# Kernel tuning notes

Measured on AMD Instinct MI355X. Metric: run time of the kernel, lower is better.

Reference implementation:

```python
import jax, jax.numpy as jnp
import numpy as np


def setup_inputs() -> dict:
    key = jax.random.key(0)
    ks = jax.random.split(key, 5)
    Bsz, T, d = 8, 2048, 1024
    x = jax.random.normal(ks[0], (Bsz, T, d), dtype=jnp.float32)
    W_in = jax.random.normal(ks[1], (d, d), dtype=jnp.float32) * (1.0 / np.sqrt(d))
    b_in = jnp.zeros((d,), dtype=jnp.float32)
    log_A = -jnp.ones((d,), dtype=jnp.float32)  # keras Constant(-1.0) init
    B_vec = jax.random.normal(ks[2], (d,), dtype=jnp.float32) * 0.05  # keras random_normal stddev
    C = jax.random.normal(ks[3], (d, d), dtype=jnp.float32) * 0.05
    D = jnp.zeros((d,), dtype=jnp.float32)
    return {"x": x, "W_in": W_in, "b_in": b_in, "log_A": log_A, "B_vec": B_vec, "C": C, "D": D}


def reference(x, W_in, b_in, log_A, B_vec, C, D):
    # u = in_proj(x)
    u = jnp.einsum('btd,de->bte', x, W_in) + b_in            # [B,T,d]
    A = -jnp.exp(log_A)                                       # [d]
    # linear recurrence h_t = h_{t-1} * A + u_t * B, h_0 = 0
    # expressed as an associative scan over pairs (a_t, b_t):
    #   (a1,b1) o (a2,b2) = (a1*a2, b1*a2 + b2)
    b = u * B_vec                                             # [B,T,d]
    a = jnp.broadcast_to(A, b.shape)                          # [B,T,d]

    def combine(e1, e2):
        a1, b1 = e1
        a2, b2 = e2
        return (a1 * a2, b1 * a2 + b2)

    _, h_seq = jax.lax.associative_scan(combine, (a, b), axis=1)  # h_t, [B,T,d]
    y = jnp.einsum('bts,sd->btd', h_seq, C)
    return y + x * D
```

## Files before the change

kernel.cpp:

```cpp
#include <hip/hip_runtime.h>
#include <hip/hip_bf16.h>

typedef unsigned short ushort_t;
typedef __bf16 bf16x8 __attribute__((ext_vector_type(8)));
typedef float f32x4 __attribute__((ext_vector_type(4)));

#define BM 128
#define BN 128
#define BK 64

__device__ __forceinline__ float bf2f(ushort_t u) {
    union { unsigned int i; float f; } x; x.i = ((unsigned int)u) << 16; return x.f;
}
__device__ __forceinline__ ushort_t f2bf(float f) {
    __hip_bfloat16 h = __float2bfloat16(f);
    return *(ushort_t*)&h;
}
__device__ __forceinline__ void async16(const void* g, void* l) {
    __builtin_amdgcn_global_load_lds((const __attribute__((address_space(1))) void*)g,
                                     (__attribute__((address_space(3))) void*)l, 16, 0, 0);
}

__global__ void prep_fused(const float* __restrict__ x, const float* __restrict__ W_in,
                           const float* __restrict__ C, const float* __restrict__ Bv,
                           __hip_bfloat16* __restrict__ xb, __hip_bfloat16* __restrict__ Wpt,
                           __hip_bfloat16* __restrict__ Ct) {
    int bid = blockIdx.x;
    if (bid < 16384) {
        size_t idx = ((size_t)bid * 256 + threadIdx.x) * 4;
        float4 v = *(const float4*)(x + idx);
        ushort4 ov;
        ov.x = f2bf(v.x); ov.y = f2bf(v.y); ov.z = f2bf(v.z); ov.w = f2bf(v.w);
        *(ushort4*)((ushort_t*)xb + idx) = ov;
        return;
    }
    __shared__ float tile[32][33];
    const float* in;
    __hip_bfloat16* out;
    bool do_scale;
    int lid;
    if (bid < 17408) { lid = bid - 16384; in = W_in; out = Wpt; do_scale = true; }
    else             { lid = bid - 17408; in = C;    out = Ct;  do_scale = false; }
    int bx = (lid & 31) * 32;
    int by = (lid >> 5) * 32;
    int tx = threadIdx.x & 31, ty = threadIdx.x >> 5;
    #pragma unroll
    for (int i = 0; i < 32; i += 8)
        tile[ty + i][tx] = in[(size_t)(by + ty + i) * 1024 + bx + tx];
    __syncthreads();
    #pragma unroll
    for (int i = 0; i < 32; i += 8) {
        int n = bx + ty + i;
        int k = by + tx;
        float s = do_scale ? Bv[n] : 1.0f;
        out[(size_t)n * 1024 + k] = __float2bfloat16(tile[tx][ty + i] * s);
    }
}

template <int EPI>
__global__ __launch_bounds__(256) void gemm_bt(
    const __hip_bfloat16* __restrict__ Ab, const __hip_bfloat16* __restrict__ Btb,
    int M, int N, int K,
    const float* __restrict__ b_in, const float* __restrict__ Bv,
    __hip_bfloat16* __restrict__ out_bf,
    const __hip_bfloat16* __restrict__ xres_bf, const float* __restrict__ Dvec,
    float* __restrict__ out_f) {
    const int tid  = threadIdx.x;
    const int wave = tid >> 6;
    const int lane = tid & 63;
    const int quad = lane >> 4;
    const int lr   = lane & 15;
    const int wm   = wave >> 1;
    const int wn   = wave & 1;

    const int lin   = blockIdx.y * gridDim.x + blockIdx.x;
    const int xcd   = lin & 7;
    const int local = lin >> 3;
    const int m_blk = xcd * 16 + (local >> 3);
    const int n_blk = local & 7;
    const int m0 = m_blk * BM;
    const int n0 = n_blk * BN;

    __shared__ __align__(16) ushort_t sA[BM * BK];
    __shared__ __align__(16) ushort_t sB[BN * BK];

    const ushort_t* A  = (const ushort_t*)Ab;
    const ushort_t* Bt = (const ushort_t*)Btb;

    f32x4 acc[4][4];
    #pragma unroll
    for (int i = 0; i < 4; ++i)
        #pragma unroll
        for (int j = 0; j < 4; ++j)
            #pragma unroll
            for (int r = 0; r < 4; ++r) acc[i][j][r] = 0.0f;

    const int row8 = lane >> 3;
    const int schunk = (lane & 7) ^ row8;
    const int ldcol = schunk * 8;
    for (int k0 = 0; k0 < K; k0 += BK) {
        __syncthreads();
        #pragma unroll
        for (int j = 0; j < 4; ++j) {
            int c = j * 4 + wave;
            int row = c * 8 + row8;
            const ushort_t* gA = A + (size_t)(m0 + row) * K + k0 + ldcol;
            async16(gA, &sA[c * 512]);
            const ushort_t* gB = Bt + (size_t)(n0 + row) * K + k0 + ldcol;
            async16(gB, &sB[c * 512]);
        }
        __syncthreads();
        #pragma unroll
        for (int kk = 0; kk < BK; kk += 32) {
            const int ck = (kk >> 3) + quad;
            const int pc = (ck ^ (lr & 7)) * 8;
            bf16x8 af[4], bfr[4];
            #pragma unroll
            for (int i = 0; i < 4; ++i)
                af[i] = *(const bf16x8*)&sA[(wm * 64 + i * 16 + lr) * BK + pc];
            #pragma unroll
            for (int j = 0; j < 4; ++j)
                bfr[j] = *(const bf16x8*)&sB[(wn * 64 + j * 16 + lr) * BK + pc];
            #pragma unroll
            for (int i = 0; i < 4; ++i)
                #pragma unroll
                for (int j = 0; j < 4; ++j)
                    acc[i][j] = __builtin_amdgcn_mfma_f32_16x16x32_bf16(af[i], bfr[j], acc[i][j], 0, 0, 0);
        }
    }

    #pragma unroll
    for (int i = 0; i < 4; ++i) {
        int row = m0 + wm * 64 + i * 16 + quad * 4;
        #pragma unroll
        for (int j = 0; j < 4; ++j) {
            int col = n0 + wn * 64 + j * 16 + lr;
            if constexpr (EPI == 0) {
                float bs = b_in[col] * Bv[col];
                #pragma unroll
                for (int r = 0; r < 4; ++r)
                    out_bf[(size_t)(row + r) * N + col] = __float2bfloat16(acc[i][j][r] + bs);
            } else {
                float dv = Dvec[col];
                #pragma unroll
                for (int r = 0; r < 4; ++r) {
                    float xv = bf2f(((const ushort_t*)xres_bf)[(size_t)(row + r) * N + col]);
                    out_f[(size_t)(row + r) * N + col] = acc[i][j][r] + xv * dv;
                }
            }
        }
    }
}

#define SCH 32
__global__ void scan_kernel(const __hip_bfloat16* __restrict__ b, __hip_bfloat16* __restrict__ h,
                            const float* __restrict__ logA, int T, int DD) {
    int c0 = (blockIdx.z * 256 + threadIdx.x) * 2;
    int q  = blockIdx.x;
    int bb = blockIdx.y;
    float2 la = *(const float2*)(logA + c0);
    float a0 = -__expf(la.x), a1 = -__expf(la.y);
    float a0_2 = a0 * a0,   a1_2 = a1 * a1;
    float a0_3 = a0_2 * a0, a1_3 = a1_2 * a1;
    float a0_4 = a0_2 * a0_2, a1_4 = a1_2 * a1_2;
    int ts = q * SCH;
    size_t base = (size_t)bb * T * DD + c0;
    float h0 = 0.f, h1 = 0.f;
    if (ts > 0) {
        const ushort_t* wp = (const ushort_t*)b + base + (size_t)(ts - 32) * DD;
        #pragma unroll
        for (int t = 0; t < 32; t += 4) {
            ushort2 v0 = *(const ushort2*)(wp);
            ushort2 v1 = *(const ushort2*)(wp + DD);
            ushort2 v2 = *(const ushort2*)(wp + 2 * (size_t)DD);
            ushort2 v3 = *(const ushort2*)(wp + 3 * (size_t)DD);
            wp += 4 * (size_t)DD;
            float s0 = fmaf(a0_3, bf2f(v0.x), fmaf(a0_2, bf2f(v1.x), fmaf(a0, bf2f(v2.x), bf2f(v3.x))));
            float s1 = fmaf(a1_3, bf2f(v0.y), fmaf(a1_2, bf2f(v1.y), fmaf(a1, bf2f(v2.y), bf2f(v3.y))));
            h0 = fmaf(a0_4, h0, s0);
            h1 = fmaf(a1_4, h1, s1);
        }
    }
    const ushort_t* bp = (const ushort_t*)b + base + (size_t)ts * DD;
    ushort_t* hp = (ushort_t*)h + base + (size_t)ts * DD;
    #pragma unroll
    for (int t = 0; t < SCH; t += 4) {
        ushort2 v0 = *(const ushort2*)(bp);
        ushort2 v1 = *(const ushort2*)(bp + DD);
        ushort2 v2 = *(const ushort2*)(bp + 2 * (size_t)DD);
        ushort2 v3 = *(const ushort2*)(bp + 3 * (size_t)DD);
        bp += 4 * (size_t)DD;
        ushort2 o;
        h0 = fmaf(a0, h0, bf2f(v0.x)); h1 = fmaf(a1, h1, bf2f(v0.y));
        o.x = f2bf(h0); o.y = f2bf(h1); *(ushort2*)hp = o;
        h0 = fmaf(a0, h0, bf2f(v1.x)); h1 = fmaf(a1, h1, bf2f(v1.y));
        o.x = f2bf(h0); o.y = f2bf(h1); *(ushort2*)(hp + DD) = o;
        h0 = fmaf(a0, h0, bf2f(v2.x)); h1 = fmaf(a1, h1, bf2f(v2.y));
        o.x = f2bf(h0); o.y = f2bf(h1); *(ushort2*)(hp + 2 * (size_t)DD) = o;
        h0 = fmaf(a0, h0, bf2f(v3.x)); h1 = fmaf(a1, h1, bf2f(v3.y));
        o.x = f2bf(h0); o.y = f2bf(h1); *(ushort2*)(hp + 3 * (size_t)DD) = o;
        hp += 4 * (size_t)DD;
    }
}

extern "C" void kernel_launch(void* const* d_in, const int* in_sizes, int n_in,
                              void* d_out, int out_size, void* d_ws, size_t ws_size,
                              hipStream_t stream) {
    const float* x    = (const float*)d_in[0];
    const float* W_in = (const float*)d_in[1];
    const float* b_in = (const float*)d_in[2];
    const float* logA = (const float*)d_in[3];
    const float* Bv   = (const float*)d_in[4];
    const float* C    = (const float*)d_in[5];
    const float* Dv   = (const float*)d_in[6];
    float* out = (float*)d_out;

    const int Bsz = 8, T = 2048, d = 1024;
    const int M = Bsz * T;

    char* w = (char*)d_ws;
    __hip_bfloat16* xb   = (__hip_bfloat16*)w;
    __hip_bfloat16* Wpt  = xb + (size_t)M * d;
    __hip_bfloat16* Ct   = Wpt + (size_t)d * d;
    __hip_bfloat16* bbuf = Ct + (size_t)d * d;
    __hip_bfloat16* hbuf = bbuf + (size_t)M * d;

    prep_fused<<<16384 + 2048, 256, 0, stream>>>(x, W_in, C, Bv, xb, Wpt, Ct);

    gemm_bt<0><<<dim3(d / BN, M / BM), 256, 0, stream>>>(
        xb, Wpt, M, d, d, b_in, Bv, bbuf, nullptr, nullptr, nullptr);
    scan_kernel<<<dim3(T / SCH, Bsz, 2), 256, 0, stream>>>(bbuf, hbuf, logA, T, d);
    gemm_bt<1><<<dim3(d / BN, M / BM), 256, 0, stream>>>(
        hbuf, Ct, M, d, d, nullptr, nullptr, nullptr, xb, Dv, out);
}
```

Measured before the change: 238.6 us.

## Pre-pack weights in MFMA fragment order and stage EPI0 stores through LDS

The prep kernel now writes the transposed weights in a packed layout that matches the MFMA B-fragment order. The GEMM then loads B fragments straight from global memory into registers and no longer stages them in LDS. The EPI==0 epilogue gathers output tiles in shared memory so it can issue coalesced 16-byte row stores instead of scattered 2-byte stores. This cuts LDS traffic and store inefficiency, but it adds uncached-by-LDS global loads of B in the inner loop and extra barriers in the epilogue.

```diff
diff --git a/kernel.cpp b/kernel.cpp
--- a/kernel.cpp
+++ b/kernel.cpp
@@ -48,18 +48,28 @@
     for (int i = 0; i < 32; i += 8)
         tile[ty + i][tx] = in[(size_t)(by + ty + i) * 1024 + bx + tx];
     __syncthreads();
-    #pragma unroll
-    for (int i = 0; i < 32; i += 8) {
-        int n = bx + ty + i;
-        int k = by + tx;
+    if (threadIdx.x < 128) {
+        int n_local = threadIdx.x & 31;
+        int quad    = threadIdx.x >> 5;
+        int n = bx + n_local;
         float s = do_scale ? Bv[n] : 1.0f;
-        out[(size_t)n * 1024 + k] = __float2bfloat16(tile[tx][ty + i] * s);
+        int lr     = n & 15;
+        int n_tile = n >> 4;
+        int k_tile = by >> 5;
+        ushort_t buf[8];
+        #pragma unroll
+        for (int j = 0; j < 8; ++j)
+            buf[j] = f2bf(tile[quad * 8 + j][n_local] * s);
+        size_t off = (((size_t)n_tile * 32 + k_tile) * 64 + quad * 16 + lr) * 8;
+        ushort_t* dst = (ushort_t*)out + off;
+        *(ushort4*)dst       = *(ushort4*)&buf[0];
+        *(ushort4*)(dst + 4) = *(ushort4*)&buf[4];
     }
 }
 
 template <int EPI>
 __global__ __launch_bounds__(256) void gemm_bt(
-    const __hip_bfloat16* __restrict__ Ab, const __hip_bfloat16* __restrict__ Btb,
+    const __hip_bfloat16* __restrict__ Ab, const __hip_bfloat16* __restrict__ Bpk,
     int M, int N, int K,
     const float* __restrict__ b_in, const float* __restrict__ Bv,
     __hip_bfloat16* __restrict__ out_bf,
@@ -82,10 +92,11 @@
     const int n0 = n_blk * BN;
 
     __shared__ __align__(16) ushort_t sA[BM * BK];
-    __shared__ __align__(16) ushort_t sB[BN * BK];
 
     const ushort_t* A  = (const ushort_t*)Ab;
-    const ushort_t* Bt = (const ushort_t*)Btb;
+    const ushort_t* Bp = (const ushort_t*)Bpk;
+    const int ktiles = K >> 5;
+    const int ntile0 = n0 >> 4;
 
     f32x4 acc[4][4];
     #pragma unroll
@@ -106,21 +117,21 @@
             int row = c * 8 + row8;
             const ushort_t* gA = A + (size_t)(m0 + row) * K + k0 + ldcol;
             async16(gA, &sA[c * 512]);
-            const ushort_t* gB = Bt + (size_t)(n0 + row) * K + k0 + ldcol;
-            async16(gB, &sB[c * 512]);
         }
         __syncthreads();
         #pragma unroll
         for (int kk = 0; kk < BK; kk += 32) {
+            const int kt = (k0 + kk) >> 5;
+            bf16x8 bfr[4];
+            #pragma unroll
+            for (int j = 0; j < 4; ++j)
+                bfr[j] = *(const bf16x8*)&Bp[((((size_t)(ntile0 + wn * 4 + j)) * ktiles + kt) * 64 + lane) * 8];
             const int ck = (kk >> 3) + quad;
             const int pc = (ck ^ (lr & 7)) * 8;
-            bf16x8 af[4], bfr[4];
+            bf16x8 af[4];
             #pragma unroll
             for (int i = 0; i < 4; ++i)
                 af[i] = *(const bf16x8*)&sA[(wm * 64 + i * 16 + lr) * BK + pc];
-            #pragma unroll
-            for (int j = 0; j < 4; ++j)
-                bfr[j] = *(const bf16x8*)&sB[(wn * 64 + j * 16 + lr) * BK + pc];
             #pragma unroll
             for (int i = 0; i < 4; ++i)
                 #pragma unroll
@@ -129,18 +140,38 @@
         }
     }
 
-    #pragma unroll
-    for (int i = 0; i < 4; ++i) {
-        int row = m0 + wm * 64 + i * 16 + quad * 4;
-        #pragma unroll
-        for (int j = 0; j < 4; ++j) {
-            int col = n0 + wn * 64 + j * 16 + lr;
-            if constexpr (EPI == 0) {
-                float bs = b_in[col] * Bv[col];
+    if constexpr (EPI == 0) {
+        ushort_t* st = sA;
+        #pragma unroll
+        for (int i = 0; i < 4; ++i) {
+            __syncthreads();
+            #pragma unroll
+            for (int j = 0; j < 4; ++j) {
+                int colL = wn * 64 + j * 16 + lr;
+                float bs = b_in[n0 + colL] * Bv[n0 + colL];
                 #pragma unroll
-                for (int r = 0; r < 4; ++r)
-                    out_bf[(size_t)(row + r) * N + col] = __float2bfloat16(acc[i][j][r] + bs);
-            } else {
+                for (int r = 0; r < 4; ++r) {
+                    int r32 = wm * 16 + quad * 4 + r;
+                    st[r32 * 136 + colL] = f2bf(acc[i][j][r] + bs);
+                }
+            }
+            __syncthreads();
+            int r32 = tid >> 3;
+            int cch = (tid & 7) * 16;
+            int row_g = m0 + (r32 >> 4) * 64 + i * 16 + (r32 & 15);
+            bf16x8 v0 = *(const bf16x8*)&st[r32 * 136 + cch];
+            bf16x8 v1 = *(const bf16x8*)&st[r32 * 136 + cch + 8];
+            ushort_t* dst = (ushort_t*)out_bf + (size_t)row_g * N + n0 + cch;
+            *(bf16x8*)dst       = v0;
+            *(bf16x8*)(dst + 8) = v1;
+        }
+    } else {
+        #pragma unroll
+        for (int i = 0; i < 4; ++i) {
+            int row = m0 + wm * 64 + i * 16 + quad * 4;
+            #pragma unroll
+            for (int j = 0; j < 4; ++j) {
+                int col = n0 + wn * 64 + j * 16 + lr;
                 float dv = Dvec[col];
                 #pragma unroll
                 for (int r = 0; r < 4; ++r) {
```

Result: slower. 245.9 us (+3.0%).
